# Kernel optimization log

Hardware: AMD Instinct MI355X
Metric: run time of the kernel (lower is better)

## Reference

```python
import jax, jax.numpy as jnp
import numpy as np

EPS = 1e-6
SLOPE = 0.25  # nn.PReLU() default init, recreated each forward -> constant slope


def conv_norm(x, W, b, g, beta):
    # 1x1 conv: [B,C,T,F] x [O,C] -> [B,O,T,F]
    y = jnp.einsum('bctf,oc->botf', x, W) + b[None, :, None, None]
    # GroupNorm(num_groups=1): normalize over (C,T,F) per sample
    mu = jnp.mean(y, axis=(1, 2, 3), keepdims=True)
    var = jnp.var(y, axis=(1, 2, 3), keepdims=True)
    y = (y - mu) * jax.lax.rsqrt(var + EPS)
    y = y * g[None, :, None, None] + beta[None, :, None, None]
    # PReLU with constant slope 0.25
    return jnp.where(y >= 0, y, SLOPE * y)


def setup_inputs() -> dict:
    key = jax.random.key(0)
    ks = jax.random.split(key, 16)
    B, C, T, F = 2, 256, 512, 128
    N, H = 4, 64
    CN = C // N
    f32 = jnp.float32

    def w(k, shape, fan_in):
        return jax.random.normal(k, shape, f32) / np.sqrt(fan_in).astype(np.float32)

    return {
        'x': jax.random.normal(ks[0], (B, C, T, F), f32),
        'Wq': w(ks[1], (N, H, C), C), 'bq': jnp.zeros((N, H), f32),
        'gq': jnp.ones((N, H), f32), 'betaq': jnp.zeros((N, H), f32),
        'Wk': w(ks[2], (N, H, C), C), 'bk': jnp.zeros((N, H), f32),
        'gk': jnp.ones((N, H), f32), 'betak': jnp.zeros((N, H), f32),
        'Wv': w(ks[3], (N, CN, C), C), 'bv': jnp.zeros((N, CN), f32),
        'gv': jnp.ones((N, CN), f32), 'betav': jnp.zeros((N, CN), f32),
        'Wp': w(ks[4], (C, C), C), 'bp': jnp.zeros((C,), f32),
        'gp': jnp.ones((C,), f32), 'betap': jnp.zeros((C,), f32),
    }


def reference(x, Wq, bq, gq, betaq, Wk, bk, gk, betak, Wv, bv, gv, betav,
              Wp, bp, gp, betap):
    B, C, T, F = x.shape
    N = Wq.shape[0]
    CN = C // N

    branch = jax.vmap(conv_norm, in_axes=(None, 0, 0, 0, 0))  # over N heads

    def to_seq(y):
        # [N,B,H,T,F] -> transpose(1,2) in torch -> [N,B,T,H,F] -> flatten(2)
        return jnp.swapaxes(y, 2, 3).reshape(y.shape[0], y.shape[1], y.shape[3], -1)

    Q = to_seq(branch(x, Wq, bq, gq, betaq))  # [N,B,T,H*F]
    K = to_seq(branch(x, Wk, bk, gk, betak))  # [N,B,T,H*F]
    V = to_seq(branch(x, Wv, bv, gv, betav))  # [N,B,T,CN*F]

    scale = 1.0 / np.sqrt(Q.shape[-1]).astype(np.float32)
    attn = jax.nn.softmax(jnp.einsum('nbtd,nbsd->nbts', Q, K) * scale, axis=-1)
    Vo = jnp.einsum('nbts,nbsd->nbtd', attn, V)  # [N,B,T,CN*F]

    # exact replication of the original reshape chain (incl. (f,t) reinterpret)
    Vo = Vo.reshape(N * B, T, CN * F)
    Vo = jnp.swapaxes(Vo, 1, 2)                    # [N*B, CN*F, T]
    Vo = Vo.reshape(N, B, CN, T, F)
    Vo = jnp.swapaxes(Vo, 0, 1).reshape(B, C, T, F)

    out = conv_norm(Vo, Wp, bp, gp, betap)
    return out + x
```

## Files before the change

### kernel.cpp

```cpp
#include <hip/hip_runtime.h>
#include <cstddef>

typedef unsigned short u16;

typedef __bf16 bf16x8 __attribute__((ext_vector_type(8)));
typedef float  f32x4  __attribute__((ext_vector_type(4)));
typedef short  s16x8  __attribute__((ext_vector_type(8)));

__device__ __forceinline__ float us2f(u16 u){
  unsigned int w = ((unsigned int)u) << 16; float f; __builtin_memcpy(&f,&w,4); return f;
}
__device__ __forceinline__ u16 f2us(float f){
  unsigned int u; __builtin_memcpy(&u,&f,4);
  u = (u + 0x7FFFu + ((u>>16)&1u)) >> 16;
  return (u16)u;
}

__device__ __forceinline__ f32x4 mfma16(bf16x8 a, bf16x8 b, f32x4 c){
  return __builtin_amdgcn_mfma_f32_16x16x32_bf16(a, b, c, 0, 0, 0);
}
__device__ __forceinline__ ushort4 pack4(f32x4 a){
  ushort4 p; p.x=f2us(a[0]); p.y=f2us(a[1]); p.z=f2us(a[2]); p.w=f2us(a[3]); return p;
}

constexpr int CC=256, CT=512, CF=128, CD=8192, CTF=65536;
constexpr float EPSV = 1e-6f;
constexpr float SLOPEV = 0.25f;
constexpr float QSCALE = 0.011048543456039806f;

#define OW_Q 0
#define OB_Q 65536
#define OG_Q 65792
#define OBE_Q 66048
#define OW_K 66304
#define OB_K 131840
#define OG_K 132096
#define OBE_K 132352
#define OW_V 132608
#define OB_V 198144
#define OG_V 198400
#define OBE_V 198656
#define OW_P 198912
#define OB_P 264448
#define OG_P 264704
#define OBE_P 264960

__global__ void k_detect(const u16* gq_raw, int* flagp){
  if (threadIdx.x==0 && blockIdx.x==0) *flagp = (gq_raw[0]==0x3F80) ? 1 : 0;
}

__global__ __launch_bounds__(256) void k_prep(
    const void* p1,const void* p2,const void* p3,const void* p4,
    const void* p5,const void* p6,const void* p7,const void* p8,
    const void* p9,const void* p10,const void* p11,const void* p12,
    const void* p13,const void* p14,const void* p15,const void* p16,
    u16* dst, const int* flagp)
{
  const void* src; int size; int off;
  switch(blockIdx.y){
    case  0: src=p1;  size=65536; off=OW_Q;  break;
    case  1: src=p2;  size=256;   off=OB_Q;  break;
    case  2: src=p3;  size=256;   off=OG_Q;  break;
    case  3: src=p4;  size=256;   off=OBE_Q; break;
    case  4: src=p5;  size=65536; off=OW_K;  break;
    case  5: src=p6;  size=256;   off=OB_K;  break;
    case  6: src=p7;  size=256;   off=OG_K;  break;
    case  7: src=p8;  size=256;   off=OBE_K; break;
    case  8: src=p9;  size=65536; off=OW_V;  break;
    case  9: src=p10; size=256;   off=OB_V;  break;
    case 10: src=p11; size=256;   off=OG_V;  break;
    case 11: src=p12; size=256;   off=OBE_V; break;
    case 12: src=p13; size=65536; off=OW_P;  break;
    case 13: src=p14; size=256;   off=OB_P;  break;
    case 14: src=p15; size=256;   off=OG_P;  break;
    default: src=p16; size=256;   off=OBE_P; break;
  }
  int idx = blockIdx.x*256 + threadIdx.x;
  if (idx >= size) return;
  u16 v;
  if (*flagp) v = ((const u16*)src)[idx];
  else        v = f2us(((const float*)src)[idx]);
  dst[off+idx] = v;
}

__global__ __launch_bounds__(256) void k_xt(const void* xin, u16* out_u16, u16* vof_ws,
                                            const int* flagp, int which, int b)
{
  const int tid = threadIdx.x;
  const int tf0 = blockIdx.x*128, c0 = blockIdx.y*128;
  const int flag = *flagp;
  __shared__ __align__(16) u16 Ts[128*136];

  if (which==0){
    const int c = tid>>1, h = tid&1;
    if (flag){
      const u16* src = (const u16*)xin + ((size_t)b<<24);
      #pragma unroll
      for (int j=0;j<8;j++){
        int tc = h*64 + j*8;
        *(s16x8*)&Ts[c*136 + tc] = *(const s16x8*)&src[(size_t)(c0+c)*CTF + tf0 + tc];
      }
    } else {
      const float* src = (const float*)xin + ((size_t)b<<24);
      #pragma unroll
      for (int j=0;j<8;j++){
        int tc = h*64 + j*8;
        float4 u0 = *(const float4*)&src[(size_t)(c0+c)*CTF + tf0 + tc];
        float4 u1 = *(const float4*)&src[(size_t)(c0+c)*CTF + tf0 + tc + 4];
        u16 tmp[8] = {f2us(u0.x),f2us(u0.y),f2us(u0.z),f2us(u0.w),
                      f2us(u1.x),f2us(u1.y),f2us(u1.z),f2us(u1.w)};
        *(s16x8*)&Ts[c*136 + tc] = *(const s16x8*)tmp;
      }
    }
  } else {
    const u16* src = (flag ? out_u16 : vof_ws) + ((size_t)b<<24);
    const int c = tid>>1, h = tid&1;
    #pragma unroll
    for (int j=0;j<8;j++){
      int tc = h*64 + j*8;
      *(s16x8*)&Ts[c*136 + tc] = *(const s16x8*)&src[(size_t)(c0+c)*CTF + tf0 + tc];
    }
  }
  __syncthreads();

  u16* dst;
  if (which==0) dst = flag ? vof_ws : (out_u16 + ((size_t)1<<25));
  else          dst = (flag ? vof_ws : out_u16) + ((size_t)b<<24);

  const int d = tid>>1, h2 = tid&1;
  #pragma unroll
  for (int j=0;j<8;j++){
    int sc = h2*64 + j*8;
    u16 tmp[8];
    #pragma unroll
    for (int i=0;i<8;i++) tmp[i] = Ts[(sc+i)*136 + d];
    *(s16x8*)&dst[(size_t)(tf0 + d)*256 + c0 + sc] = *(const s16x8*)tmp;
  }
}

__global__ __launch_bounds__(256) void k_conv(
    const u16* xt_a, const u16* xt_b, const u16* wtsb,
    u16* qn, u16* kn, u16* vn,
    float* stats, const int* flagp, int n, int b0)
{
  const int tid = threadIdx.x;
  const int t   = blockIdx.x;
  const u16* xt = (*flagp) ? xt_a : xt_b;

  const int l = tid & 63, w = tid >> 6;
  const int lr = l & 15, kg = l >> 4;

  __shared__ __align__(16) u16 Ys[64*136];
  __shared__ float wred[3][4][2];

  bf16x8 a[2][8];
  #pragma unroll
  for (int i=0;i<2;i++){
    const u16* ar = xt + (size_t)(t*128 + w*32 + i*16 + lr)*256 + 8*kg;
    #pragma unroll
    for (int d=0;d<8;d++) a[i][d] = *(const bf16x8*)(ar + d*32);
  }

  for (int br=0; br<3; ++br){
    const u16* W    = wtsb + (br==0?OW_Q: br==1?OW_K:OW_V) + n*64*256;
    const u16* bias = wtsb + (br==0?OB_Q: br==1?OB_K:OB_V) + n*64;
    u16* yo = (br==0? qn : (br==1? kn : vn));
    f32x4 acc[2][4];
    #pragma unroll
    for (int j=0;j<4;j++){
      float bb = us2f(bias[j*16+lr]);
      acc[0][j] = (f32x4){bb,bb,bb,bb};
      acc[1][j] = (f32x4){bb,bb,bb,bb};
    }
    #pragma unroll
    for (int d=0; d<8; ++d){
      #pragma unroll
      for (int j=0;j<4;j++){
        bf16x8 bfr = *(const bf16x8*)(W + (size_t)(j*16+lr)*256 + 8*kg + d*32);
        acc[0][j] = mfma16(a[0][d], bfr, acc[0][j]);
        acc[1][j] = mfma16(a[1][d], bfr, acc[1][j]);
      }
    }
    float s=0.f, s2=0.f;
    #pragma unroll
    for (int i=0;i<2;i++)
      #pragma unroll
      for (int j=0;j<4;j++)
        #pragma unroll
        for (int ii=0;ii<4;ii++){ float v = acc[i][j][ii]; s += v; s2 += v*v; }
    #pragma unroll
    for (int m=1; m<64; m<<=1){ s += __shfl_xor(s,m); s2 += __shfl_xor(s2,m); }
    if (l==0){ wred[br][w][0]=s; wred[br][w][1]=s2; }
    __syncthreads();
    #pragma unroll
    for (int i=0;i<2;i++)
      #pragma unroll
      for (int j=0;j<4;j++)
        *(ushort4*)&Ys[(j*16+lr)*136 + (w*32 + i*16 + 4*kg)] = pack4(acc[i][j]);
    __syncthreads();
    #pragma unroll
    for (int k2=0;k2<4;k2++){
      int idx = tid + k2*256;
      int o = idx >> 4, f8 = (idx & 15)*8;
      *(s16x8*)&yo[(size_t)t*CD + o*CF + f8] = *(const s16x8*)&Ys[o*136 + f8];
    }
  }
  __syncthreads();
  if (tid < 3){
    float s  = wred[tid][0][0]+wred[tid][1][0]+wred[tid][2][0]+wred[tid][3][0];
    float s2 = wred[tid][0][1]+wred[tid][1][1]+wred[tid][2][1]+wred[tid][3][1];
    int g = tid*8 + n*2 + b0;
    atomicAdd(&stats[2*g],   s);
    atomicAdd(&stats[2*g+1], s2);
  }
}

__global__ __launch_bounds__(256) void k_norm(
    u16* q, u16* k, const u16* wtsb,
    const float* stats, int n, int b0)
{
  const int br = blockIdx.y;
  u16* y = (br==0? q : k);
  const u16* g  = wtsb + (br==0?OG_Q : OG_K ) + n*64;
  const u16* be = wtsb + (br==0?OBE_Q: OBE_K) + n*64;
  size_t idx0 = ((size_t)blockIdx.x*256 + threadIdx.x)*8;
  int ch = (int)((idx0 >> 7) & 63);
  int grp = br*8 + n*2 + b0;
  float sm = stats[2*grp], sq = stats[2*grp+1];
  const float Minv = 1.0f/4194304.0f;
  float mean = sm*Minv;
  float var  = fmaxf(sq*Minv - mean*mean, 0.0f);
  float rs = rsqrtf(var + EPSV);
  float gg = us2f(g[ch]) * rs;
  float bb = us2f(be[ch]);
  float sc = (br==0)? QSCALE : 1.0f;
  ushort4 u0 = *(const ushort4*)&y[idx0];
  ushort4 u1 = *(const ushort4*)&y[idx0+4];
  float vals[8] = {us2f(u0.x),us2f(u0.y),us2f(u0.z),us2f(u0.w),
                   us2f(u1.x),us2f(u1.y),us2f(u1.z),us2f(u1.w)};
  #pragma unroll
  for (int j=0;j<8;j++){
    float t = (vals[j]-mean)*gg + bb;
    t = (t>=0.f)? t : SLOPEV*t;
    vals[j] = t*sc;
  }
  ushort4 o0, o1;
  o0.x=f2us(vals[0]); o0.y=f2us(vals[1]); o0.z=f2us(vals[2]); o0.w=f2us(vals[3]);
  o1.x=f2us(vals[4]); o1.y=f2us(vals[5]); o1.z=f2us(vals[6]); o1.w=f2us(vals[7]);
  *(ushort4*)&y[idx0]   = o0;
  *(ushort4*)&y[idx0+4] = o1;
}

__global__ __launch_bounds__(512) void k_qk(const u16* __restrict__ qm,
                                            const u16* __restrict__ km,
                                            float* __restrict__ S)
{
  const int tid = threadIdx.x;
  const int l   = tid & 63;
  const int w   = tid >> 6;
  const int lr  = l & 15;
  const int kg  = l >> 4;
  const int s0  = blockIdx.x*32;
  const int t0  = blockIdx.y*32;

  const u16* qp = qm + (size_t)(t0 + lr)*CD + w*1024 + 8*kg;
  const u16* kp = km + (size_t)(s0 + lr)*CD + w*1024 + 8*kg;

  f32x4 acc00 = {0.f,0.f,0.f,0.f};
  f32x4 acc01 = acc00, acc10 = acc00, acc11 = acc00;

  #pragma unroll 4
  for (int d=0; d<1024; d+=32){
    bf16x8 a0 = *(const bf16x8*)(qp + d);
    bf16x8 a1 = *(const bf16x8*)(qp + d + 16*CD);
    bf16x8 b0 = *(const bf16x8*)(kp + d);
    bf16x8 b1 = *(const bf16x8*)(kp + d + 16*CD);
    acc00 = mfma16(a0, b0, acc00);
    acc01 = mfma16(a0, b1, acc01);
    acc10 = mfma16(a1, b0, acc10);
    acc11 = mfma16(a1, b1, acc11);
  }

  __shared__ float Sb[8][32][36];
  #pragma unroll
  for (int ii=0; ii<4; ++ii){
    Sb[w][4*kg+ii][lr]       = acc00[ii];
    Sb[w][4*kg+ii][lr+16]    = acc01[ii];
    Sb[w][16+4*kg+ii][lr]    = acc10[ii];
    Sb[w][16+4*kg+ii][lr+16] = acc11[ii];
  }
  __syncthreads();
  #pragma unroll
  for (int rep=0; rep<2; ++rep){
    int idx = tid + rep*512;
    int tt = idx >> 5, ss = idx & 31;
    float v = 0.f;
    #pragma unroll
    for (int ww=0; ww<8; ++ww) v += Sb[ww][tt][ss];
    S[(size_t)(t0+tt)*CT + s0 + ss] = v;
  }
}

__global__ __launch_bounds__(256) void k_vtn(const u16* __restrict__ v,
                                             u16* __restrict__ vt,
                                             const u16* wtsb,
                                             const float* stats, int n, int b0)
{
  const int tid = threadIdx.x;
  const int d0 = blockIdx.x*128, s0 = blockIdx.y*128;
  __shared__ __align__(16) u16 Ts[128*136];
  {
    const int sA = tid>>1, h = tid&1;
    #pragma unroll
    for (int j=0;j<8;j++){
      int dc = h*64 + j*8;
      *(s16x8*)&Ts[sA*136 + dc] = *(const s16x8*)&v[(size_t)(s0+sA)*CD + d0 + dc];
    }
  }
  __syncthreads();
  const int dl = tid>>1, h2 = tid&1;
  const int ch = (d0 + dl) >> 7;
  const int grp = 16 + n*2 + b0;
  float sm = stats[2*grp], sq = stats[2*grp+1];
  const float Minv = 1.0f/4194304.0f;
  float mean = sm*Minv;
  float var  = fmaxf(sq*Minv - mean*mean, 0.0f);
  float rs = rsqrtf(var + EPSV);
  float gg = us2f(wtsb[OG_V  + n*64 + ch]) * rs;
  float bb = us2f(wtsb[OBE_V + n*64 + ch]);
  #pragma unroll
  for (int j=0;j<8;j++){
    int sc = h2*64 + j*8;
    u16 tmp[8];
    #pragma unroll
    for (int i=0;i<8;i++){
      float val = us2f(Ts[(sc+i)*136 + dl]);
      float t = (val-mean)*gg + bb;
      t = (t>=0.f)? t : SLOPEV*t;
      tmp[i] = f2us(t);
    }
    *(s16x8*)&vt[(size_t)(d0+dl)*CT + s0 + sc] = *(const s16x8*)tmp;
  }
}

__global__ __launch_bounds__(256) void k_softmax(const float* S, u16* P)
{
  const int row = blockIdx.x;
  const int tid = threadIdx.x;
  const float* Sr = S + (size_t)row*CT;
  u16* Pr = P + (size_t)row*1024;
  float a = Sr[tid], c = Sr[tid+256];
  __shared__ float buf[256];
  float m = fmaxf(a,c);
  buf[tid] = m;
  __syncthreads();
  for (int w=128; w; w>>=1){
    if (tid<w) buf[tid] = fmaxf(buf[tid], buf[tid+w]);
    __syncthreads();
  }
  m = buf[0];
  __syncthreads();
  float e0 = __expf(a-m), e1 = __expf(c-m);
  buf[tid] = e0+e1;
  __syncthreads();
  for (int w=128; w; w>>=1){
    if (tid<w) buf[tid] += buf[tid+w];
    __syncthreads();
  }
  float r = 1.0f/buf[0];
  Pr[tid]     = f2us(e0*r);
  Pr[tid+256] = f2us(e1*r);
}

__global__ __launch_bounds__(256) void k_pv(const u16* __restrict__ P,
                                            const u16* __restrict__ vt,
                                            u16* out_u16, u16* vof_ws,
                                            const int* flagp, int n, int b0)
{
  const int tid = threadIdx.x;
  const int l = tid & 63, w = tid >> 6;
  const int lr = l & 15, kg = l >> 4;
  const int dv0 = blockIdx.x*64;
  const int t00 = blockIdx.y*256;
  const int tb  = t00 + w*64;

  const u16* ap0 = P  + (size_t)(tb + lr)*1024 + 8*kg;
  const u16* bp0 = vt + (size_t)(dv0 + lr)*CT  + 8*kg;

  f32x4 acc[4][4];
  #pragma unroll
  for (int i=0;i<4;i++)
    #pragma unroll
    for (int j=0;j<4;j++) acc[i][j] = (f32x4){0.f,0.f,0.f,0.f};

  for (int s=0; s<CT; s+=32){
    bf16x8 av[4], bv[4];
    #pragma unroll
    for (int i=0;i<4;i++) av[i] = *(const bf16x8*)(ap0 + (size_t)i*16*1024 + s);
    #pragma unroll
    for (int j=0;j<4;j++) bv[j] = *(const bf16x8*)(bp0 + (size_t)j*16*CT + s);
    #pragma unroll
    for (int i=0;i<4;i++)
      #pragma unroll
      for (int j=0;j<4;j++)
        acc[i][j] = mfma16(av[i], bv[j], acc[i][j]);
  }

  __shared__ __align__(16) u16 Ot[64*264];
  #pragma unroll
  for (int i=0;i<4;i++)
    #pragma unroll
    for (int j=0;j<4;j++)
      *(ushort4*)&Ot[(j*16+lr)*264 + (w*64 + i*16 + 4*kg)] = pack4(acc[i][j]);
  __syncthreads();

  u16* vof = (*flagp) ? out_u16 : vof_ws;
  #pragma unroll
  for (int k2=0;k2<8;k2++){
    int idx = tid + k2*256;
    int r = idx >> 5, t8 = (idx & 31)*8;
    int dv = dv0 + r, cn = dv >> 7, f = dv & 127;
    *(s16x8*)&vof[((size_t)(b0*CC + n*64 + cn))*CTF + (size_t)f*CT + t00 + t8] =
        *(const s16x8*)&Ot[r*264 + t8];
  }
}

__global__ __launch_bounds__(256) void k_proj(u16* out_u16, u16* vof_ws,
                                              const int* flagp,
                                              const u16* wtsb,
                                              float* stats)
{
  const int tid = threadIdx.x;
  const int tf0 = blockIdx.x*256;
  const int b   = blockIdx.y;
  const int flag = *flagp;
  const u16* vtT = (flag ? vof_ws : out_u16) + ((size_t)b<<24);
  u16* yb        = (flag ? out_u16 : vof_ws) + ((size_t)b<<24);

  __shared__ __align__(16) u16 Ys[64*264];
  __shared__ float wredp[4][2];
  const int l = tid&63, w = tid>>6, lr = l&15, kg = l>>4;
  float ts=0.f, ts2=0.f;

  for (int oc=0; oc<4; ++oc){
    const int o0c = oc*64;
    f32x4 acc[4][4];
    #pragma unroll
    for (int j=0;j<4;j++){
      float bb = us2f(wtsb[OB_P + o0c + j*16 + lr]);
      #pragma unroll
      for (int i=0;i<4;i++) acc[i][j] = (f32x4){bb,bb,bb,bb};
    }
    #pragma unroll
    for (int d=0; d<8; ++d){
      bf16x8 av[4];
      #pragma unroll
      for (int i=0;i<4;i++)
        av[i] = *(const bf16x8*)(vtT + (size_t)(tf0 + w*64 + i*16 + lr)*256 + 8*kg + d*32);
      #pragma unroll
      for (int j=0;j<4;j++){
        bf16x8 bfr = *(const bf16x8*)(wtsb + OW_P + (size_t)(o0c + j*16 + lr)*256 + 8*kg + d*32);
        #pragma unroll
        for (int i=0;i<4;i++) acc[i][j] = mfma16(av[i], bfr, acc[i][j]);
      }
    }
    #pragma unroll
    for (int i=0;i<4;i++)
      #pragma unroll
      for (int j=0;j<4;j++)
        #pragma unroll
        for (int ii=0;ii<4;ii++){ float v = acc[i][j][ii]; ts += v; ts2 += v*v; }
    __syncthreads();
    #pragma unroll
    for (int i=0;i<4;i++)
      #pragma unroll
      for (int j=0;j<4;j++)
        *(ushort4*)&Ys[(j*16+lr)*264 + (w*64 + i*16 + 4*kg)] = pack4(acc[i][j]);
    __syncthreads();
    #pragma unroll
    for (int k2=0;k2<8;k2++){
      int idx = tid + k2*256;
      int o = idx >> 5, t8 = (idx & 31)*8;
      *(s16x8*)&yb[(size_t)(o0c + o)*CTF + tf0 + t8] = *(const s16x8*)&Ys[o*264 + t8];
    }
  }
  #pragma unroll
  for (int m=1; m<64; m<<=1){ ts += __shfl_xor(ts,m); ts2 += __shfl_xor(ts2,m); }
  if (l==0){ wredp[w][0]=ts; wredp[w][1]=ts2; }
  __syncthreads();
  if (tid==0){
    float s  = wredp[0][0]+wredp[1][0]+wredp[2][0]+wredp[3][0];
    float s2 = wredp[0][1]+wredp[1][1]+wredp[2][1]+wredp[3][1];
    atomicAdd(&stats[2*(24+b)],   s);
    atomicAdd(&stats[2*(24+b)+1], s2);
  }
}

__global__ __launch_bounds__(256) void k_final(void* dout, const void* x,
                                               const u16* vof_ws, const int* flagp,
                                               const u16* wtsb,
                                               const float* stats)
{
  const int flag = *flagp;
  size_t idx0 = ((size_t)blockIdx.x*256 + threadIdx.x)*8;
  int b = (int)(idx0 >> 24);
  int c = (int)((idx0 >> 16) & 255);
  float sm = stats[2*(24+b)], sq = stats[2*(24+b)+1];
  const float Minv = 1.0f/16777216.0f;
  float mean = sm*Minv;
  float var  = fmaxf(sq*Minv - mean*mean, 0.0f);
  float rs = rsqrtf(var + EPSV);
  float gg = us2f(wtsb[OG_P + c])*rs, bb = us2f(wtsb[OBE_P + c]);

  const u16* yp = flag ? (const u16*)dout : vof_ws;
  ushort4 u0 = *(const ushort4*)&yp[idx0];
  ushort4 u1 = *(const ushort4*)&yp[idx0+4];
  float vy[8] = {us2f(u0.x),us2f(u0.y),us2f(u0.z),us2f(u0.w),
                 us2f(u1.x),us2f(u1.y),us2f(u1.z),us2f(u1.w)};
  float vx[8];
  if (flag){
    const u16* xb = (const u16*)x;
    ushort4 x0 = *(const ushort4*)&xb[idx0];
    ushort4 x1 = *(const ushort4*)&xb[idx0+4];
    vx[0]=us2f(x0.x); vx[1]=us2f(x0.y); vx[2]=us2f(x0.z); vx[3]=us2f(x0.w);
    vx[4]=us2f(x1.x); vx[5]=us2f(x1.y); vx[6]=us2f(x1.z); vx[7]=us2f(x1.w);
  } else {
    const float* xf = (const float*)x;
    float4 x0 = *(const float4*)&xf[idx0];
    float4 x1 = *(const float4*)&xf[idx0+4];
    vx[0]=x0.x; vx[1]=x0.y; vx[2]=x0.z; vx[3]=x0.w;
    vx[4]=x1.x; vx[5]=x1.y; vx[6]=x1.z; vx[7]=x1.w;
  }
  #pragma unroll
  for (int j=0;j<8;j++){
    float t = (vy[j]-mean)*gg + bb;
    t = (t>=0.f)? t : SLOPEV*t;
    vy[j] = t + vx[j];
  }
  if (flag){
    u16* ob = (u16*)dout;
    ushort4 o0, o1;
    o0.x=f2us(vy[0]); o0.y=f2us(vy[1]); o0.z=f2us(vy[2]); o0.w=f2us(vy[3]);
    o1.x=f2us(vy[4]); o1.y=f2us(vy[5]); o1.z=f2us(vy[6]); o1.w=f2us(vy[7]);
    *(ushort4*)&ob[idx0]   = o0;
    *(ushort4*)&ob[idx0+4] = o1;
  } else {
    float* of = (float*)dout;
    *(float4*)&of[idx0]   = make_float4(vy[0],vy[1],vy[2],vy[3]);
    *(float4*)&of[idx0+4] = make_float4(vy[4],vy[5],vy[6],vy[7]);
  }
}

extern "C" void kernel_launch(void* const* d_in, const int* in_sizes, int n_in,
                              void* d_out, int out_size, void* d_ws, size_t ws_size,
                              hipStream_t stream)
{
  (void)in_sizes; (void)n_in; (void)out_size; (void)ws_size;
  char* ws = (char*)d_ws;
  int* flagp    = (int*)ws;
  float* stats  = (float*)(ws + 16);
  u16* wtsb     = (u16*)(ws + 512);
  u16* qn       = (u16*)(ws + 532480);
  u16* kn       = (u16*)(ws + 8921088);
  u16* vn       = (u16*)(ws + 17309696);
  float* Sn     = (float*)(ws + 25698304);
  u16* vof_ws   = (u16*)(ws + 27262976);
  u16* out_u16  = (u16*)d_out;

  hipMemsetAsync(stats, 0, 256, stream);
  k_detect<<<1,64,0,stream>>>((const u16*)d_in[3], flagp);
  k_prep<<<dim3(256,16),256,0,stream>>>(d_in[1],d_in[2],d_in[3],d_in[4],
                                        d_in[5],d_in[6],d_in[7],d_in[8],
                                        d_in[9],d_in[10],d_in[11],d_in[12],
                                        d_in[13],d_in[14],d_in[15],d_in[16],
                                        wtsb, flagp);
  for (int b0=0; b0<2; ++b0){
    k_xt<<<dim3(512,2),256,0,stream>>>(d_in[0], out_u16, vof_ws, flagp, 0, b0);
    for (int n=0; n<4; ++n){
      k_conv<<<512,256,0,stream>>>(vof_ws, out_u16 + ((size_t)1<<25), wtsb,
                                   qn,kn,vn, stats, flagp, n, b0);
      k_norm<<<dim3(2048,2),256,0,stream>>>(qn,kn, wtsb, stats, n, b0);
      k_qk<<<dim3(16,16),512,0,stream>>>(qn,kn,Sn);
      k_vtn<<<dim3(64,4),256,0,stream>>>(vn, qn, wtsb, stats, n, b0);
      k_softmax<<<512,256,0,stream>>>(Sn,(u16*)Sn);
      k_pv<<<dim3(128,2),256,0,stream>>>((const u16*)Sn, qn, out_u16, vof_ws, flagp, n, b0);
    }
  }
  k_xt<<<dim3(512,2),256,0,stream>>>(d_in[0], out_u16, vof_ws, flagp, 1, 0);
  k_xt<<<dim3(512,2),256,0,stream>>>(d_in[0], out_u16, vof_ws, flagp, 1, 1);
  k_proj<<<dim3(256,2),256,0,stream>>>(out_u16, vof_ws, flagp, wtsb, stats);
  k_final<<<16384,256,0,stream>>>(d_out, d_in[0], vof_ws, flagp, wtsb, stats);
}
```

Baseline: 1.398 ms.

## Retile QK with reduced split-K, fuse V-transpose with softmax, retile projection

The QK kernel now uses 64x64 output tiles per block with only a 2-way reduction split instead of 8-way, which cuts the shared-memory reduction and lets more warps write results directly. The V normalize/transpose and softmax kernels are merged into one launch with a block-index dispatch to save a launch and let both run together. The projection kernel uses smaller 64-token tiles with activations held in registers across output chunks, quadrupling the grid. The risk is that the QK grid shrinks to 64 blocks, which may underfill the GPU.

```diff
diff --git a/kernel.cpp b/kernel.cpp
--- a/kernel.cpp
+++ b/kernel.cpp
@@ -260,17 +260,20 @@
   const int w   = tid >> 6;
   const int lr  = l & 15;
   const int kg  = l >> 4;
-  const int s0  = blockIdx.x*32;
-  const int t0  = blockIdx.y*32;
-
-  const u16* qp = qm + (size_t)(t0 + lr)*CD + w*1024 + 8*kg;
-  const u16* kp = km + (size_t)(s0 + lr)*CD + w*1024 + 8*kg;
+  const int wk  = w >> 2;
+  const int wy  = (w >> 1) & 1;
+  const int wx  = w & 1;
+  const int t0  = blockIdx.y*64 + wy*32;
+  const int s0  = blockIdx.x*64 + wx*32;
+
+  const u16* qp = qm + (size_t)(t0 + lr)*CD + wk*4096 + 8*kg;
+  const u16* kp = km + (size_t)(s0 + lr)*CD + wk*4096 + 8*kg;
 
   f32x4 acc00 = {0.f,0.f,0.f,0.f};
   f32x4 acc01 = acc00, acc10 = acc00, acc11 = acc00;
 
   #pragma unroll 4
-  for (int d=0; d<1024; d+=32){
+  for (int d=0; d<4096; d+=32){
     bf16x8 a0 = *(const bf16x8*)(qp + d);
     bf16x8 a1 = *(const bf16x8*)(qp + d + 16*CD);
     bf16x8 b0 = *(const bf16x8*)(kp + d);
@@ -281,95 +284,101 @@
     acc11 = mfma16(a1, b1, acc11);
   }
 
-  __shared__ float Sb[8][32][36];
-  #pragma unroll
-  for (int ii=0; ii<4; ++ii){
-    Sb[w][4*kg+ii][lr]       = acc00[ii];
-    Sb[w][4*kg+ii][lr+16]    = acc01[ii];
-    Sb[w][16+4*kg+ii][lr]    = acc10[ii];
-    Sb[w][16+4*kg+ii][lr+16] = acc11[ii];
+  __shared__ float Sb[4][32][36];
+  const int q4 = wy*2 + wx;
+  if (wk==1){
+    #pragma unroll
+    for (int ii=0; ii<4; ++ii){
+      Sb[q4][4*kg+ii][lr]       = acc00[ii];
+      Sb[q4][4*kg+ii][lr+16]    = acc01[ii];
+      Sb[q4][16+4*kg+ii][lr]    = acc10[ii];
+      Sb[q4][16+4*kg+ii][lr+16] = acc11[ii];
+    }
   }
   __syncthreads();
-  #pragma unroll
-  for (int rep=0; rep<2; ++rep){
-    int idx = tid + rep*512;
-    int tt = idx >> 5, ss = idx & 31;
-    float v = 0.f;
-    #pragma unroll
-    for (int ww=0; ww<8; ++ww) v += Sb[ww][tt][ss];
-    S[(size_t)(t0+tt)*CT + s0 + ss] = v;
-  }
-}
-
-__global__ __launch_bounds__(256) void k_vtn(const u16* __restrict__ v,
-                                             u16* __restrict__ vt,
-                                             const u16* wtsb,
-                                             const float* stats, int n, int b0)
-{
+  if (wk==0){
+    const int sA = s0 + lr, sB = sA + 16;
+    #pragma unroll
+    for (int ii=0; ii<4; ++ii){
+      int tA = t0 + 4*kg + ii;
+      int tB = tA + 16;
+      S[(size_t)tA*CT + sA] = acc00[ii] + Sb[q4][4*kg+ii][lr];
+      S[(size_t)tA*CT + sB] = acc01[ii] + Sb[q4][4*kg+ii][lr+16];
+      S[(size_t)tB*CT + sA] = acc10[ii] + Sb[q4][16+4*kg+ii][lr];
+      S[(size_t)tB*CT + sB] = acc11[ii] + Sb[q4][16+4*kg+ii][lr+16];
+    }
+  }
+}
+
+__global__ __launch_bounds__(256) void k_vs(const u16* __restrict__ v,
+                                            u16* __restrict__ vt,
+                                            const u16* wtsb,
+                                            const float* stats, int n, int b0,
+                                            float* S, u16* P)
+{
+  __shared__ __align__(16) u16 Ts[128*136];
   const int tid = threadIdx.x;
-  const int d0 = blockIdx.x*128, s0 = blockIdx.y*128;
-  __shared__ __align__(16) u16 Ts[128*136];
-  {
-    const int sA = tid>>1, h = tid&1;
+  const int bid = blockIdx.x;
+  if (bid < 256){
+    const int d0 = (bid>>2)*128, s0 = (bid&3)*128;
+    {
+      const int sA = tid>>1, h = tid&1;
+      #pragma unroll
+      for (int j=0;j<8;j++){
+        int dc = h*64 + j*8;
+        *(s16x8*)&Ts[sA*136 + dc] = *(const s16x8*)&v[(size_t)(s0+sA)*CD + d0 + dc];
+      }
+    }
+    __syncthreads();
+    const int dl = tid>>1, h2 = tid&1;
+    const int ch = (d0 + dl) >> 7;
+    const int grp = 16 + n*2 + b0;
+    float sm = stats[2*grp], sq = stats[2*grp+1];
+    const float Minv = 1.0f/4194304.0f;
+    float mean = sm*Minv;
+    float var  = fmaxf(sq*Minv - mean*mean, 0.0f);
+    float rs = rsqrtf(var + EPSV);
+    float gg = us2f(wtsb[OG_V  + n*64 + ch]) * rs;
+    float bb = us2f(wtsb[OBE_V + n*64 + ch]);
     #pragma unroll
     for (int j=0;j<8;j++){
-      int dc = h*64 + j*8;
-      *(s16x8*)&Ts[sA*136 + dc] = *(const s16x8*)&v[(size_t)(s0+sA)*CD + d0 + dc];
-    }
-  }
-  __syncthreads();
-  const int dl = tid>>1, h2 = tid&1;
-  const int ch = (d0 + dl) >> 7;
-  const int grp = 16 + n*2 + b0;
-  float sm = stats[2*grp], sq = stats[2*grp+1];
-  const float Minv = 1.0f/4194304.0f;
-  float mean = sm*Minv;
-  float var  = fmaxf(sq*Minv - mean*mean, 0.0f);
-  float rs = rsqrtf(var + EPSV);
-  float gg = us2f(wtsb[OG_V  + n*64 + ch]) * rs;
-  float bb = us2f(wtsb[OBE_V + n*64 + ch]);
-  #pragma unroll
-  for (int j=0;j<8;j++){
-    int sc = h2*64 + j*8;
-    u16 tmp[8];
-    #pragma unroll
-    for (int i=0;i<8;i++){
-      float val = us2f(Ts[(sc+i)*136 + dl]);
-      float t = (val-mean)*gg + bb;
-      t = (t>=0.f)? t : SLOPEV*t;
-      tmp[i] = f2us(t);
-    }
-    *(s16x8*)&vt[(size_t)(d0+dl)*CT + s0 + sc] = *(const s16x8*)tmp;
-  }
-}
-
-__global__ __launch_bounds__(256) void k_softmax(const float* S, u16* P)
-{
-  const int row = blockIdx.x;
-  const int tid = threadIdx.x;
-  const float* Sr = S + (size_t)row*CT;
-  u16* Pr = P + (size_t)row*1024;
-  float a = Sr[tid], c = Sr[tid+256];
-  __shared__ float buf[256];
-  float m = fmaxf(a,c);
-  buf[tid] = m;
-  __syncthreads();
-  for (int w=128; w; w>>=1){
-    if (tid<w) buf[tid] = fmaxf(buf[tid], buf[tid+w]);
-    __syncthreads();
-  }
-  m = buf[0];
-  __syncthreads();
-  float e0 = __expf(a-m), e1 = __expf(c-m);
-  buf[tid] = e0+e1;
-  __syncthreads();
-  for (int w=128; w; w>>=1){
-    if (tid<w) buf[tid] += buf[tid+w];
-    __syncthreads();
-  }
-  float r = 1.0f/buf[0];
-  Pr[tid]     = f2us(e0*r);
-  Pr[tid+256] = f2us(e1*r);
+      int sc = h2*64 + j*8;
+      u16 tmp[8];
+      #pragma unroll
+      for (int i=0;i<8;i++){
+        float val = us2f(Ts[(sc+i)*136 + dl]);
+        float t = (val-mean)*gg + bb;
+        t = (t>=0.f)? t : SLOPEV*t;
+        tmp[i] = f2us(t);
+      }
+      *(s16x8*)&vt[(size_t)(d0+dl)*CT + s0 + sc] = *(const s16x8*)tmp;
+    }
+  } else {
+    float* buf = (float*)Ts;
+    const int row = bid - 256;
+    const float* Sr = S + (size_t)row*CT;
+    u16* Pr = P + (size_t)row*1024;
+    float a = Sr[tid], c = Sr[tid+256];
+    float m = fmaxf(a,c);
+    buf[tid] = m;
+    __syncthreads();
+    for (int w=128; w; w>>=1){
+      if (tid<w) buf[tid] = fmaxf(buf[tid], buf[tid+w]);
+      __syncthreads();
+    }
+    m = buf[0];
+    __syncthreads();
+    float e0 = __expf(a-m), e1 = __expf(c-m);
+    buf[tid] = e0+e1;
+    __syncthreads();
+    for (int w=128; w; w>>=1){
+      if (tid<w) buf[tid] += buf[tid+w];
+      __syncthreads();
+    }
+    float r = 1.0f/buf[0];
+    Pr[tid]     = f2us(e0*r);
+    Pr[tid+256] = f2us(e1*r);
+  }
 }
 
 __global__ __launch_bounds__(256) void k_pv(const u16* __restrict__ P,
@@ -431,58 +440,57 @@
                                               float* stats)
 {
   const int tid = threadIdx.x;
-  const int tf0 = blockIdx.x*256;
+  const int tf0 = blockIdx.x*64;
   const int b   = blockIdx.y;
   const int flag = *flagp;
   const u16* vtT = (flag ? vof_ws : out_u16) + ((size_t)b<<24);
   u16* yb        = (flag ? out_u16 : vof_ws) + ((size_t)b<<24);
 
-  __shared__ __align__(16) u16 Ys[64*264];
+  const int l = tid&63, w = tid>>6, lr = l&15, kg = l>>4;
+
+  bf16x8 a[8];
+  {
+    const u16* ar = vtT + (size_t)(tf0 + w*16 + lr)*256 + 8*kg;
+    #pragma unroll
+    for (int d=0;d<8;d++) a[d] = *(const bf16x8*)(ar + d*32);
+  }
+
+  __shared__ __align__(16) u16 Ys[64][72];
   __shared__ float wredp[4][2];
-  const int l = tid&63, w = tid>>6, lr = l&15, kg = l>>4;
   float ts=0.f, ts2=0.f;
 
   for (int oc=0; oc<4; ++oc){
     const int o0c = oc*64;
-    f32x4 acc[4][4];
+    f32x4 acc[4];
     #pragma unroll
     for (int j=0;j<4;j++){
       float bb = us2f(wtsb[OB_P + o0c + j*16 + lr]);
-      #pragma unroll
-      for (int i=0;i<4;i++) acc[i][j] = (f32x4){bb,bb,bb,bb};
+      acc[j] = (f32x4){bb,bb,bb,bb};
     }
     #pragma unroll
     for (int d=0; d<8; ++d){
-      bf16x8 av[4];
-      #pragma unroll
-      for (int i=0;i<4;i++)
-        av[i] = *(const bf16x8*)(vtT + (size_t)(tf0 + w*64 + i*16 + lr)*256 + 8*kg + d*32);
       #pragma unroll
       for (int j=0;j<4;j++){
         bf16x8 bfr = *(const bf16x8*)(wtsb + OW_P + (size_t)(o0c + j*16 + lr)*256 + 8*kg + d*32);
-        #pragma unroll
-        for (int i=0;i<4;i++) acc[i][j] = mfma16(av[i], bfr, acc[i][j]);
+        acc[j] = mfma16(a[d], bfr, acc[j]);
       }
     }
     #pragma unroll
-    for (int i=0;i<4;i++)
-      #pragma unroll
-      for (int j=0;j<4;j++)
-        #pragma unroll
-        for (int ii=0;ii<4;ii++){ float v = acc[i][j][ii]; ts += v; ts2 += v*v; }
-    __syncthreads();
-    #pragma unroll
-    for (int i=0;i<4;i++)
-      #pragma unroll
-      for (int j=0;j<4;j++)
-        *(ushort4*)&Ys[(j*16+lr)*264 + (w*64 + i*16 + 4*kg)] = pack4(acc[i][j]);
-    __syncthreads();
-    #pragma unroll
-    for (int k2=0;k2<8;k2++){
-      int idx = tid + k2*256;
-      int o = idx >> 5, t8 = (idx & 31)*8;
-      *(s16x8*)&yb[(size_t)(o0c + o)*CTF + tf0 + t8] = *(const s16x8*)&Ys[o*264 + t8];
-    }
+    for (int j=0;j<4;j++)
+      #pragma unroll
+      for (int ii=0;ii<4;ii++){ float v = acc[j][ii]; ts += v; ts2 += v*v; }
+    __syncthreads();
+    #pragma unroll
+    for (int j=0;j<4;j++)
+      *(ushort4*)&Ys[j*16+lr][w*16 + 4*kg] = pack4(acc[j]);
+    __syncthreads();
+    {
+      int o = tid>>2, t8 = (tid&3)*16;
+      size_t adr = (size_t)(o0c + o)*CTF + tf0 + t8;
+      *(s16x8*)&yb[adr]     = *(const s16x8*)&Ys[o][t8];
+      *(s16x8*)&yb[adr + 8] = *(const s16x8*)&Ys[o][t8+8];
+    }
+    __syncthreads();
   }
   #pragma unroll
   for (int m=1; m<64; m<<=1){ ts += __shfl_xor(ts,m); ts2 += __shfl_xor(ts2,m); }
@@ -580,14 +588,13 @@
       k_conv<<<512,256,0,stream>>>(vof_ws, out_u16 + ((size_t)1<<25), wtsb,
                                    qn,kn,vn, stats, flagp, n, b0);
       k_norm<<<dim3(2048,2),256,0,stream>>>(qn,kn, wtsb, stats, n, b0);
-      k_qk<<<dim3(16,16),512,0,stream>>>(qn,kn,Sn);
-      k_vtn<<<dim3(64,4),256,0,stream>>>(vn, qn, wtsb, stats, n, b0);
-      k_softmax<<<512,256,0,stream>>>(Sn,(u16*)Sn);
+      k_qk<<<dim3(8,8),512,0,stream>>>(qn,kn,Sn);
+      k_vs<<<768,256,0,stream>>>(vn, qn, wtsb, stats, n, b0, Sn, (u16*)Sn);
       k_pv<<<dim3(128,2),256,0,stream>>>((const u16*)Sn, qn, out_u16, vof_ws, flagp, n, b0);
     }
   }
   k_xt<<<dim3(512,2),256,0,stream>>>(d_in[0], out_u16, vof_ws, flagp, 1, 0);
   k_xt<<<dim3(512,2),256,0,stream>>>(d_in[0], out_u16, vof_ws, flagp, 1, 1);
-  k_proj<<<dim3(256,2),256,0,stream>>>(out_u16, vof_ws, flagp, wtsb, stats);
+  k_proj<<<dim3(1024,2),256,0,stream>>>(out_u16, vof_ws, flagp, wtsb, stats);
   k_final<<<16384,256,0,stream>>>(d_out, d_in[0], vof_ws, flagp, wtsb, stats);
 }
```

Result: slower. 2.142 ms (+53.2%).
